# Kernel optimization log

Hardware: AMD Instinct MI355X
Metric: run time of the kernel (lower is better)

## Reference

```python
import jax, jax.numpy as jnp
import numpy as np

NUM_LAGS_P1 = 4
N_NODES = 2048


def setup_inputs() -> dict:
    key = jax.random.key(0)
    # Scale so that ||A*A||_1 ~ O(1): entries ~ N(0, s^2), A_sq entries ~ s^2,
    # row sums of A_sq ~ n*s^2. s = 0.02 -> n*s^2 ~ 0.82 for n=2048.
    scale = 0.02
    adjacencies = scale * jax.random.normal(
        key, (NUM_LAGS_P1, N_NODES, N_NODES), dtype=jnp.float32
    )
    return {"adjacencies": adjacencies}


def reference(adjacencies) -> jnp.ndarray:
    # Only the contemporaneous slice A_0 needs the acyclicity constraint.
    A = adjacencies[0]                     # [n, n]
    n = A.shape[0]
    A_sq = A * A                           # elementwise square (NOTEARS h(A))
    E = jax.scipy.linalg.expm(A_sq)        # Pade + scaling-and-squaring
    h = jnp.trace(E) - n                   # scalar constraint value
    return h
```

## Files before the change

### kernel.cpp

```cpp
#include <hip/hip_runtime.h>
#include <hip/hip_bf16.h>

#define NN 2048
typedef unsigned short us;
typedef __attribute__((ext_vector_type(8))) short short8;
typedef __attribute__((ext_vector_type(4))) float f4;
typedef __attribute__((ext_vector_type(4))) float f32x4;
typedef __attribute__((ext_vector_type(8))) unsigned short us8;

__device__ __forceinline__ us f2bf(float f) {
    unsigned int u = __float_as_uint(f);
    u += 0x7fffu + ((u >> 16) & 1u);
    return (us)(u >> 16);
}
__device__ __forceinline__ float bf2f(us h) {
    return __uint_as_float(((unsigned int)h) << 16);
}
__device__ __forceinline__ void gload16(const us* g, us* l) {
    __builtin_amdgcn_global_load_lds(
        (const __attribute__((address_space(1))) unsigned int*)g,
        (__attribute__((address_space(3))) unsigned int*)l, 16, 0, 0);
}

__global__ void prep_kernel(const float* __restrict__ A0,
                            us* __restrict__ Bbf, us* __restrict__ BbfT,
                            float* __restrict__ rs, float* __restrict__ cs,
                            double* __restrict__ pt1) {
    __shared__ float sq[64][65];
    const int I = blockIdx.y, J = blockIdx.x;
    const int tid = threadIdx.x, lane = tid & 63, wv = tid >> 6;
    const size_t rI = (size_t)I * 64, rJ = (size_t)J * 64;

    #pragma unroll
    for (int u = tid; u < 512; u += 256) {
        const int row = u >> 3, c8 = (u & 7) * 8;
        f4 a0 = *(const f4*)&A0[(rI + row) * NN + rJ + c8];
        f4 a1 = *(const f4*)&A0[(rI + row) * NN + rJ + c8 + 4];
        us8 o;
        #pragma unroll
        for (int k = 0; k < 4; ++k) { float s = a0[k] * a0[k]; sq[row][c8 + k] = s; o[k] = f2bf(s); }
        #pragma unroll
        for (int k = 0; k < 4; ++k) { float s = a1[k] * a1[k]; sq[row][c8 + 4 + k] = s; o[4 + k] = f2bf(s); }
        *(us8*)&Bbf[(rI + row) * NN + rJ + c8] = o;
    }
    __syncthreads();

    #pragma unroll
    for (int u = tid; u < 512; u += 256) {
        const int r = u >> 3, c0 = (u & 7) * 8;
        us8 o;
        #pragma unroll
        for (int k = 0; k < 8; ++k) o[k] = f2bf(sq[c0 + k][r]);
        *(us8*)&BbfT[(rJ + r) * NN + rI + c0] = o;
    }

    if (I == J) {
        if (tid < 64) { rs[rI + tid] = 0.f; cs[rI + tid] = 0.f; }
        if (wv == 0) {
            double t1 = sq[lane][lane];
            #pragma unroll
            for (int s = 32; s > 0; s >>= 1) t1 += __shfl_down(t1, s, 64);
            if (lane == 0) pt1[I] = t1;
        }
    }
}

__launch_bounds__(256, 2)
__global__ void gemm_kernel(const us* __restrict__ A, const us* __restrict__ BT,
                            us* __restrict__ c2a, us* __restrict__ c2b,
                            float* __restrict__ rs, float* __restrict__ cs) {
    __shared__ us lA[2][4096];
    __shared__ us lB[2][4096];
    const int tid  = threadIdx.x;
    const int lane = tid & 63;
    const int w    = tid >> 6;
    const int wr   = w >> 1, wc = w & 1;
    const int rowBase = blockIdx.y * 128;
    const int colBase = blockIdx.x * 128;
    const int kbase   = blockIdx.z * 1024;
    us* __restrict__ C = blockIdx.z ? c2b : c2a;
    const int lr = lane & 15;
    const int lk = (lane >> 4) * 8;

    const int srow = tid >> 2;
    const int scol = (tid & 3) * 8;
    const us* gA0 = A  + (size_t)(rowBase + srow) * NN + kbase + scol;
    const us* gA1 = A  + (size_t)(rowBase + 64 + srow) * NN + kbase + scol;
    const us* gB0 = BT + (size_t)(colBase + srow) * NN + kbase + scol;
    const us* gB1 = BT + (size_t)(colBase + 64 + srow) * NN + kbase + scol;
    const int d0 = srow * 32 + scol;
    const int d1 = (64 + srow) * 32 + scol;

    f32x4 acc[4][4] = {};

    gload16(gA0, &lA[0][d0]);
    gload16(gA1, &lA[0][d1]);
    gload16(gB0, &lB[0][d0]);
    gload16(gB1, &lB[0][d1]);
    __syncthreads();

    for (int t = 0; t < 32; ++t) {
        const int cur = t & 1;
        if (t < 31) {
            const int k = (t + 1) * 32;
            gload16(gA0 + k, &lA[cur ^ 1][d0]);
            gload16(gA1 + k, &lA[cur ^ 1][d1]);
            gload16(gB0 + k, &lB[cur ^ 1][d0]);
            gload16(gB1 + k, &lB[cur ^ 1][d1]);
        }
        short8 af[4], bfr[4];
        #pragma unroll
        for (int mi = 0; mi < 4; ++mi)
            af[mi] = *(const short8*)&lA[cur][(wr * 64 + mi * 16 + lr) * 32 + lk];
        #pragma unroll
        for (int ni = 0; ni < 4; ++ni)
            bfr[ni] = *(const short8*)&lB[cur][(wc * 64 + ni * 16 + lr) * 32 + lk];
        #pragma unroll
        for (int mi = 0; mi < 4; ++mi)
            #pragma unroll
            for (int ni = 0; ni < 4; ++ni)
                acc[mi][ni] = __builtin_amdgcn_mfma_f32_16x16x32_bf16(
                    af[mi], bfr[ni], acc[mi][ni], 0, 0, 0);
        __syncthreads();
    }

    const int orow = (lane >> 4) * 4;
    const int ocol = lane & 15;
    float colp[4] = {0.f, 0.f, 0.f, 0.f};
    #pragma unroll
    for (int mi = 0; mi < 4; ++mi) {
        #pragma unroll
        for (int r = 0; r < 4; ++r) {
            const int gr = rowBase + wr * 64 + mi * 16 + orow + r;
            float rowp = 0.f;
            #pragma unroll
            for (int ni = 0; ni < 4; ++ni) {
                float v = acc[mi][ni][r];
                C[(size_t)gr * NN + colBase + wc * 64 + ni * 16 + ocol] = f2bf(v);
                rowp += v;
                colp[ni] += v;
            }
            rowp += __shfl_xor(rowp, 1, 64);
            rowp += __shfl_xor(rowp, 2, 64);
            rowp += __shfl_xor(rowp, 4, 64);
            rowp += __shfl_xor(rowp, 8, 64);
            if ((lane & 15) == 0) atomicAdd(&rs[gr], rowp);
        }
    }
    #pragma unroll
    for (int ni = 0; ni < 4; ++ni) {
        colp[ni] += __shfl_xor(colp[ni], 16, 64);
        colp[ni] += __shfl_xor(colp[ni], 32, 64);
        if (lane < 16) atomicAdd(&cs[colBase + wc * 64 + ni * 16 + ocol], colp[ni]);
    }
}

__global__ void corr_kernel(const us* __restrict__ c2a, const us* __restrict__ c2b,
                            const us* __restrict__ Bbf, const us* __restrict__ BbfT,
                            double* __restrict__ pt2, double* __restrict__ pt3,
                            double* __restrict__ pt4) {
    __shared__ float cT[64][65];
    __shared__ double wred[3][4];
    const int I = blockIdx.y, J = blockIdx.x;
    const int tid = threadIdx.x, lane = tid & 63, wv = tid >> 6;
    const size_t rI = (size_t)I * 64, rJ = (size_t)J * 64;

    double t2 = 0, t3 = 0;
    float myC[2][8];
    #pragma unroll
    for (int ph = 0; ph < 2; ++ph) {
        const int u = tid + ph * 256;
        const int row = u >> 3, c8 = (u & 7) * 8;
        const size_t off  = (rI + row) * NN + rJ + c8;
        const size_t off2 = (rJ + row) * NN + rI + c8;
        us8 va = *(const us8*)&c2a[off];
        us8 vb = *(const us8*)&c2b[off];
        us8 vt = *(const us8*)&BbfT[off];
        us8 vf = *(const us8*)&Bbf[off];
        us8 wa = *(const us8*)&c2a[off2];
        us8 wb = *(const us8*)&c2b[off2];
        #pragma unroll
        for (int k = 0; k < 8; ++k) {
            float c = bf2f(va[k]) + bf2f(vb[k]);
            myC[ph][k] = c;
            t3 += (double)(c * bf2f(vt[k]));
            t2 += (double)(bf2f(vf[k]) * bf2f(vt[k]));
            cT[row][c8 + k] = bf2f(wa[k]) + bf2f(wb[k]);
        }
    }
    __syncthreads();

    double t4 = 0;
    #pragma unroll
    for (int ph = 0; ph < 2; ++ph) {
        const int u = tid + ph * 256;
        const int row = u >> 3, c8 = (u & 7) * 8;
        #pragma unroll
        for (int k = 0; k < 8; ++k)
            t4 += (double)(myC[ph][k] * cT[c8 + k][row]);
    }

    #pragma unroll
    for (int s = 32; s > 0; s >>= 1) {
        t2 += __shfl_down(t2, s, 64);
        t3 += __shfl_down(t3, s, 64);
        t4 += __shfl_down(t4, s, 64);
    }
    if (lane == 0) { wred[0][wv] = t2; wred[1][wv] = t3; wred[2][wv] = t4; }
    __syncthreads();
    if (tid == 0) {
        const int b = blockIdx.y * 32 + blockIdx.x;
        pt2[b] = wred[0][0] + wred[0][1] + wred[0][2] + wred[0][3];
        pt3[b] = wred[1][0] + wred[1][1] + wred[1][2] + wred[1][3];
        pt4[b] = wred[2][0] + wred[2][1] + wred[2][2] + wred[2][3];
    }
}

__global__ void finalize_kernel(const float* __restrict__ rs,
                                const float* __restrict__ cs,
                                const double* __restrict__ pt1,
                                const double* __restrict__ pt2,
                                const double* __restrict__ pt3,
                                const double* __restrict__ pt4,
                                float* __restrict__ out) {
    __shared__ double red[256];
    const int t = threadIdx.x;
    double t1 = 0, t2 = 0, t3 = 0, t4 = 0, s2 = 0, s4 = 0;
    if (t < 32) t1 = pt1[t];
    for (int i = t; i < 1024; i += 256) { t2 += pt2[i]; t3 += pt3[i]; t4 += pt4[i]; }
    for (int i = t; i < NN; i += 256) {
        double r = rs[i];
        s2 += r; s4 += r * (double)cs[i];
    }
    double vals[6] = {t1, t2, t3, t4, s2, s4};
    double tot[6];
    for (int v = 0; v < 6; ++v) {
        red[t] = vals[v]; __syncthreads();
        for (int s = 128; s > 0; s >>= 1) { if (t < s) red[t] += red[t + s]; __syncthreads(); }
        tot[v] = red[0]; __syncthreads();
    }
    if (t == 0) {
        double lam2 = tot[5] / tot[4];
        double lam  = sqrt(lam2);
        double tail = exp(lam) - 1.0 - lam - lam2 * 0.5
                      - lam * lam2 * (1.0 / 6.0) - lam2 * lam2 * (1.0 / 24.0);
        out[0] = (float)(tot[0] + tot[1] * 0.5 + tot[2] * (1.0 / 6.0)
                         + tot[3] * (1.0 / 24.0) + tail);
    }
}

extern "C" void kernel_launch(void* const* d_in, const int* in_sizes, int n_in,
                              void* d_out, int out_size, void* d_ws, size_t ws_size,
                              hipStream_t stream) {
    const float* A0 = (const float*)d_in[0];
    char* ws = (char*)d_ws;
    us*     Bbf  = (us*)(ws);
    us*     BbfT = (us*)(ws + 8388608);
    us*     c2a  = (us*)(ws + 16777216);
    us*     c2b  = (us*)(ws + 25165824);
    float*  rs   = (float*)(ws + 33554432);
    float*  cs   = (float*)(ws + 33562624);
    double* pt1  = (double*)(ws + 33570816);
    double* pt2  = (double*)(ws + 33571328);
    double* pt3  = (double*)(ws + 33579520);
    double* pt4  = (double*)(ws + 33587712);
    float*  out  = (float*)d_out;

    prep_kernel<<<dim3(32, 32), 256, 0, stream>>>(A0, Bbf, BbfT, rs, cs, pt1);
    gemm_kernel<<<dim3(16, 16, 2), 256, 0, stream>>>(Bbf, BbfT, c2a, c2b, rs, cs);
    corr_kernel<<<dim3(32, 32), 256, 0, stream>>>(c2a, c2b, Bbf, BbfT, pt2, pt3, pt4);
    finalize_kernel<<<1, 256, 0, stream>>>(rs, cs, pt1, pt2, pt3, pt4, out);
}
```

Before: 139.5 us.

## Split GEMM K into four slices, single-buffer LDS, fold trace(B^2) into GEMM epilogue

The GEMM split-K factor goes from 2 to 4, giving 1024 blocks instead of 512. The LDS double buffering is dropped so more blocks fit per CU (launch bounds raised to 4). The tr(B^2) term is now taken from the diagonal of the GEMM output through a double atomic, instead of rereading Bbf in the correction kernel. The cost is more partial-product traffic: four bf16 partial matrices to write and reread. The single-buffered loop also serialises loads and MFMA within each block.

Measured after the change: 148.9 us. 6.7% more time.

```diff
diff --git a/kernel.cpp b/kernel.cpp
--- a/kernel.cpp
+++ b/kernel.cpp
@@ -25,7 +25,7 @@
 __global__ void prep_kernel(const float* __restrict__ A0,
                             us* __restrict__ Bbf, us* __restrict__ BbfT,
                             float* __restrict__ rs, float* __restrict__ cs,
-                            double* __restrict__ pt1) {
+                            double* __restrict__ pt1, double* __restrict__ accs) {
     __shared__ float sq[64][65];
     const int I = blockIdx.y, J = blockIdx.x;
     const int tid = threadIdx.x, lane = tid & 63, wv = tid >> 6;
@@ -56,6 +56,7 @@
 
     if (I == J) {
         if (tid < 64) { rs[rI + tid] = 0.f; cs[rI + tid] = 0.f; }
+        if (I == 0 && tid == 64) accs[0] = 0.0;
         if (wv == 0) {
             double t1 = sq[lane][lane];
             #pragma unroll
@@ -65,20 +66,20 @@
     }
 }
 
-__launch_bounds__(256, 2)
+__launch_bounds__(256, 4)
 __global__ void gemm_kernel(const us* __restrict__ A, const us* __restrict__ BT,
-                            us* __restrict__ c2a, us* __restrict__ c2b,
-                            float* __restrict__ rs, float* __restrict__ cs) {
-    __shared__ us lA[2][4096];
-    __shared__ us lB[2][4096];
+                            us* __restrict__ c2, float* __restrict__ rs,
+                            float* __restrict__ cs, double* __restrict__ accs) {
+    __shared__ us lA[4096];
+    __shared__ us lB[4096];
     const int tid  = threadIdx.x;
     const int lane = tid & 63;
     const int w    = tid >> 6;
     const int wr   = w >> 1, wc = w & 1;
     const int rowBase = blockIdx.y * 128;
     const int colBase = blockIdx.x * 128;
-    const int kbase   = blockIdx.z * 1024;
-    us* __restrict__ C = blockIdx.z ? c2b : c2a;
+    const int kbase   = blockIdx.z * 512;
+    us* __restrict__ C = c2 + (size_t)blockIdx.z * (NN * (size_t)NN);
     const int lr = lane & 15;
     const int lk = (lane >> 4) * 8;
 
@@ -93,28 +94,21 @@
 
     f32x4 acc[4][4] = {};
 
-    gload16(gA0, &lA[0][d0]);
-    gload16(gA1, &lA[0][d1]);
-    gload16(gB0, &lB[0][d0]);
-    gload16(gB1, &lB[0][d1]);
-    __syncthreads();
-
-    for (int t = 0; t < 32; ++t) {
-        const int cur = t & 1;
-        if (t < 31) {
-            const int k = (t + 1) * 32;
-            gload16(gA0 + k, &lA[cur ^ 1][d0]);
-            gload16(gA1 + k, &lA[cur ^ 1][d1]);
-            gload16(gB0 + k, &lB[cur ^ 1][d0]);
-            gload16(gB1 + k, &lB[cur ^ 1][d1]);
-        }
+    for (int t = 0; t < 16; ++t) {
+        const int k = t * 32;
+        gload16(gA0 + k, &lA[d0]);
+        gload16(gA1 + k, &lA[d1]);
+        gload16(gB0 + k, &lB[d0]);
+        gload16(gB1 + k, &lB[d1]);
+        __syncthreads();
+
         short8 af[4], bfr[4];
         #pragma unroll
         for (int mi = 0; mi < 4; ++mi)
-            af[mi] = *(const short8*)&lA[cur][(wr * 64 + mi * 16 + lr) * 32 + lk];
+            af[mi] = *(const short8*)&lA[(wr * 64 + mi * 16 + lr) * 32 + lk];
         #pragma unroll
         for (int ni = 0; ni < 4; ++ni)
-            bfr[ni] = *(const short8*)&lB[cur][(wc * 64 + ni * 16 + lr) * 32 + lk];
+            bfr[ni] = *(const short8*)&lB[(wc * 64 + ni * 16 + lr) * 32 + lk];
         #pragma unroll
         for (int mi = 0; mi < 4; ++mi)
             #pragma unroll
@@ -126,6 +120,8 @@
 
     const int orow = (lane >> 4) * 4;
     const int ocol = lane & 15;
+    const bool diagblk = (rowBase == colBase);
+    double tdiag = 0.0;
     float colp[4] = {0.f, 0.f, 0.f, 0.f};
     #pragma unroll
     for (int mi = 0; mi < 4; ++mi) {
@@ -136,9 +132,11 @@
             #pragma unroll
             for (int ni = 0; ni < 4; ++ni) {
                 float v = acc[mi][ni][r];
-                C[(size_t)gr * NN + colBase + wc * 64 + ni * 16 + ocol] = f2bf(v);
+                const int gc = colBase + wc * 64 + ni * 16 + ocol;
+                C[(size_t)gr * NN + gc] = f2bf(v);
                 rowp += v;
                 colp[ni] += v;
+                if (diagblk && gr == gc) tdiag += (double)v;
             }
             rowp += __shfl_xor(rowp, 1, 64);
             rowp += __shfl_xor(rowp, 2, 64);
@@ -153,19 +151,24 @@
         colp[ni] += __shfl_xor(colp[ni], 32, 64);
         if (lane < 16) atomicAdd(&cs[colBase + wc * 64 + ni * 16 + ocol], colp[ni]);
     }
-}
-
-__global__ void corr_kernel(const us* __restrict__ c2a, const us* __restrict__ c2b,
-                            const us* __restrict__ Bbf, const us* __restrict__ BbfT,
-                            double* __restrict__ pt2, double* __restrict__ pt3,
-                            double* __restrict__ pt4) {
+    if (diagblk) {
+        #pragma unroll
+        for (int s = 32; s > 0; s >>= 1) tdiag += __shfl_down(tdiag, s, 64);
+        if (lane == 0 && tdiag != 0.0) atomicAdd(&accs[0], tdiag);
+    }
+}
+
+__global__ void corr_kernel(const us* __restrict__ c2,
+                            const us* __restrict__ BbfT,
+                            double* __restrict__ pt3, double* __restrict__ pt4) {
     __shared__ float cT[64][65];
-    __shared__ double wred[3][4];
+    __shared__ double wred[2][4];
+    const size_t PS = (size_t)NN * NN;
     const int I = blockIdx.y, J = blockIdx.x;
     const int tid = threadIdx.x, lane = tid & 63, wv = tid >> 6;
     const size_t rI = (size_t)I * 64, rJ = (size_t)J * 64;
 
-    double t2 = 0, t3 = 0;
+    double t3 = 0;
     float myC[2][8];
     #pragma unroll
     for (int ph = 0; ph < 2; ++ph) {
@@ -173,19 +176,21 @@
         const int row = u >> 3, c8 = (u & 7) * 8;
         const size_t off  = (rI + row) * NN + rJ + c8;
         const size_t off2 = (rJ + row) * NN + rI + c8;
-        us8 va = *(const us8*)&c2a[off];
-        us8 vb = *(const us8*)&c2b[off];
+        us8 v0 = *(const us8*)&c2[off];
+        us8 v1 = *(const us8*)&c2[off + PS];
+        us8 v2 = *(const us8*)&c2[off + 2 * PS];
+        us8 v3 = *(const us8*)&c2[off + 3 * PS];
         us8 vt = *(const us8*)&BbfT[off];
-        us8 vf = *(const us8*)&Bbf[off];
-        us8 wa = *(const us8*)&c2a[off2];
-        us8 wb = *(const us8*)&c2b[off2];
+        us8 w0 = *(const us8*)&c2[off2];
+        us8 w1 = *(const us8*)&c2[off2 + PS];
+        us8 w2 = *(const us8*)&c2[off2 + 2 * PS];
+        us8 w3 = *(const us8*)&c2[off2 + 3 * PS];
         #pragma unroll
         for (int k = 0; k < 8; ++k) {
-            float c = bf2f(va[k]) + bf2f(vb[k]);
+            float c = (bf2f(v0[k]) + bf2f(v1[k])) + (bf2f(v2[k]) + bf2f(v3[k]));
             myC[ph][k] = c;
             t3 += (double)(c * bf2f(vt[k]));
-            t2 += (double)(bf2f(vf[k]) * bf2f(vt[k]));
-            cT[row][c8 + k] = bf2f(wa[k]) + bf2f(wb[k]);
+            cT[row][c8 + k] = (bf2f(w0[k]) + bf2f(w1[k])) + (bf2f(w2[k]) + bf2f(w3[k]));
         }
     }
     __syncthreads();
@@ -202,50 +207,49 @@
 
     #pragma unroll
     for (int s = 32; s > 0; s >>= 1) {
-        t2 += __shfl_down(t2, s, 64);
         t3 += __shfl_down(t3, s, 64);
         t4 += __shfl_down(t4, s, 64);
     }
-    if (lane == 0) { wred[0][wv] = t2; wred[1][wv] = t3; wred[2][wv] = t4; }
+    if (lane == 0) { wred[0][wv] = t3; wred[1][wv] = t4; }
     __syncthreads();
     if (tid == 0) {
         const int b = blockIdx.y * 32 + blockIdx.x;
-        pt2[b] = wred[0][0] + wred[0][1] + wred[0][2] + wred[0][3];
-        pt3[b] = wred[1][0] + wred[1][1] + wred[1][2] + wred[1][3];
-        pt4[b] = wred[2][0] + wred[2][1] + wred[2][2] + wred[2][3];
+        pt3[b] = wred[0][0] + wred[0][1] + wred[0][2] + wred[0][3];
+        pt4[b] = wred[1][0] + wred[1][1] + wred[1][2] + wred[1][3];
     }
 }
 
 __global__ void finalize_kernel(const float* __restrict__ rs,
                                 const float* __restrict__ cs,
                                 const double* __restrict__ pt1,
-                                const double* __restrict__ pt2,
+                                const double* __restrict__ accs,
                                 const double* __restrict__ pt3,
                                 const double* __restrict__ pt4,
                                 float* __restrict__ out) {
     __shared__ double red[256];
     const int t = threadIdx.x;
-    double t1 = 0, t2 = 0, t3 = 0, t4 = 0, s2 = 0, s4 = 0;
+    double t1 = 0, t3 = 0, t4 = 0, s2 = 0, s4 = 0;
     if (t < 32) t1 = pt1[t];
-    for (int i = t; i < 1024; i += 256) { t2 += pt2[i]; t3 += pt3[i]; t4 += pt4[i]; }
+    for (int i = t; i < 1024; i += 256) { t3 += pt3[i]; t4 += pt4[i]; }
     for (int i = t; i < NN; i += 256) {
         double r = rs[i];
         s2 += r; s4 += r * (double)cs[i];
     }
-    double vals[6] = {t1, t2, t3, t4, s2, s4};
-    double tot[6];
-    for (int v = 0; v < 6; ++v) {
+    double vals[5] = {t1, t3, t4, s2, s4};
+    double tot[5];
+    for (int v = 0; v < 5; ++v) {
         red[t] = vals[v]; __syncthreads();
         for (int s = 128; s > 0; s >>= 1) { if (t < s) red[t] += red[t + s]; __syncthreads(); }
         tot[v] = red[0]; __syncthreads();
     }
     if (t == 0) {
-        double lam2 = tot[5] / tot[4];
+        double t2 = accs[0];
+        double lam2 = tot[4] / tot[3];
         double lam  = sqrt(lam2);
         double tail = exp(lam) - 1.0 - lam - lam2 * 0.5
                       - lam * lam2 * (1.0 / 6.0) - lam2 * lam2 * (1.0 / 24.0);
-        out[0] = (float)(tot[0] + tot[1] * 0.5 + tot[2] * (1.0 / 6.0)
-                         + tot[3] * (1.0 / 24.0) + tail);
+        out[0] = (float)(tot[0] + t2 * 0.5 + tot[1] * (1.0 / 6.0)
+                         + tot[2] * (1.0 / 24.0) + tail);
     }
 }
 
@@ -256,18 +260,17 @@
     char* ws = (char*)d_ws;
     us*     Bbf  = (us*)(ws);
     us*     BbfT = (us*)(ws + 8388608);
-    us*     c2a  = (us*)(ws + 16777216);
-    us*     c2b  = (us*)(ws + 25165824);
-    float*  rs   = (float*)(ws + 33554432);
-    float*  cs   = (float*)(ws + 33562624);
-    double* pt1  = (double*)(ws + 33570816);
-    double* pt2  = (double*)(ws + 33571328);
-    double* pt3  = (double*)(ws + 33579520);
-    double* pt4  = (double*)(ws + 33587712);
+    us*     c2   = (us*)(ws + 16777216);
+    float*  rs   = (float*)(ws + 50331648);
+    float*  cs   = (float*)(ws + 50339840);
+    double* pt1  = (double*)(ws + 50348032);
+    double* accs = (double*)(ws + 50348544);
+    double* pt3  = (double*)(ws + 50349056);
+    double* pt4  = (double*)(ws + 50357248);
     float*  out  = (float*)d_out;
 
-    prep_kernel<<<dim3(32, 32), 256, 0, stream>>>(A0, Bbf, BbfT, rs, cs, pt1);
-    gemm_kernel<<<dim3(16, 16, 2), 256, 0, stream>>>(Bbf, BbfT, c2a, c2b, rs, cs);
-    corr_kernel<<<dim3(32, 32), 256, 0, stream>>>(c2a, c2b, Bbf, BbfT, pt2, pt3, pt4);
-    finalize_kernel<<<1, 256, 0, stream>>>(rs, cs, pt1, pt2, pt3, pt4, out);
-}
+    prep_kernel<<<dim3(32, 32), 256, 0, stream>>>(A0, Bbf, BbfT, rs, cs, pt1, accs);
+    gemm_kernel<<<dim3(16, 16, 4), 256, 0, stream>>>(Bbf, BbfT, c2, rs, cs, accs);
+    corr_kernel<<<dim3(32, 32), 256, 0, stream>>>(c2, BbfT, pt3, pt4);
+    finalize_kernel<<<1, 256, 0, stream>>>(rs, cs, pt1, accs, pt3, pt4, out);
+}
```
